# Performance work log

Measured on AMD Instinct MI355X. Metric: run time of the kernel, lower is better.

The kernel has to match this reference:

```python
import jax, jax.numpy as jnp
import numpy as np
import math

B, L = 4, 2048
D_MODEL, N_HEADS, D_K, D_V, D_FF, FACTOR = 512, 8, 64, 64, 2048, 5


def _layernorm(x, g, b, eps=1e-5):
    m = x.mean(-1, keepdims=True)
    v = jnp.mean((x - m) ** 2, axis=-1, keepdims=True)
    return (x - m) * jax.lax.rsqrt(v + eps) * g + b


def setup_inputs() -> dict:
    key = jax.random.key(0)
    ks = jax.random.split(key, 8)
    w = lambda k, shape: (jax.random.normal(k, shape, jnp.float32) * 0.02)
    sample_k = min(FACTOR * int(math.ceil(math.log(L))), L)  # c*ln(L_K) sampled keys per query
    return {
        "x": jax.random.normal(ks[0], (B, L, D_MODEL), jnp.float32),
        "Wq": w(ks[1], (D_MODEL, N_HEADS * D_K)),
        "Wk": w(ks[2], (D_MODEL, N_HEADS * D_K)),
        "Wv": w(ks[3], (D_MODEL, N_HEADS * D_V)),
        "Wo": w(ks[4], (N_HEADS * D_V, D_MODEL)),
        "ln1_g": jnp.ones((D_MODEL,), jnp.float32),
        "ln1_b": jnp.zeros((D_MODEL,), jnp.float32),
        "conv1_w": w(ks[5], (D_FF, D_MODEL)),
        "conv1_b": jnp.zeros((D_FF,), jnp.float32),
        "conv2_w": w(ks[6], (D_MODEL, D_FF)),
        "conv2_b": jnp.zeros((D_MODEL,), jnp.float32),
        "ln2_g": jnp.ones((D_MODEL,), jnp.float32),
        "ln2_b": jnp.zeros((D_MODEL,), jnp.float32),
        # Informer samples sample_k random keys per query position (constant indices)
        "sample_idx": jax.random.randint(ks[7], (L, sample_k), 0, L),
    }


def reference(x, Wq, Wk, Wv, Wo, ln1_g, ln1_b, conv1_w, conv1_b, conv2_w, conv2_b, ln2_g, ln2_b, sample_idx):
    Bx, Lx, D = x.shape
    H = N_HEADS
    # projections -> [B,H,L,d]
    Q = (x @ Wq).reshape(Bx, Lx, H, D_K).transpose(0, 2, 1, 3)
    K = (x @ Wk).reshape(Bx, Lx, H, D_K).transpose(0, 2, 1, 3)
    V = (x @ Wv).reshape(Bx, Lx, H, D_V).transpose(0, 2, 1, 3)

    u = min(FACTOR * int(math.ceil(math.log(Lx))), Lx)  # top-u active queries
    # sampled QK scores: [B,H,L,sample_k]
    K_samp = K[:, :, sample_idx]                              # [B,H,L,S,dk]
    qk_s = jnp.einsum('bhle,bhlse->bhls', Q, K_samp)
    # sparsity measure M = max - mean (Informer divides sum by L_K)
    M = qk_s.max(-1) - qk_s.sum(-1) / Lx                      # [B,H,L]
    _, top = jax.lax.top_k(M, u)                              # [B,H,u]

    Q_red = jnp.take_along_axis(Q, top[..., None], axis=2)    # [B,H,u,dk]
    scores = jnp.einsum('bhue,bhle->bhul', Q_red, K) / math.sqrt(D_K)
    attn = jax.nn.softmax(scores, axis=-1)                    # [B,H,u,L]

    # initial context = mean of V over keys; update only top-u query rows
    ctx = jnp.broadcast_to(V.mean(axis=2, keepdims=True), V.shape)  # [B,H,L,dv]
    upd = jnp.einsum('bhul,bhld->bhud', attn, V)              # [B,H,u,dv]
    bi = jnp.arange(Bx)[:, None, None]
    hi = jnp.arange(H)[None, :, None]
    ctx = ctx.at[bi, hi, top].set(upd)

    out = ctx.transpose(0, 2, 1, 3).reshape(Bx, Lx, H * D_V) @ Wo
    x1 = _layernorm(x + out, ln1_g, ln1_b)  # residual + norm inside attention sublayer

    # conv1d(k=1) FFN == per-token linear; dropout is identity in eval
    y = jax.nn.gelu(x1 @ conv1_w.T + conv1_b, approximate=False)
    y = y @ conv2_w.T + conv2_b
    return _layernorm(x1 + y, ln2_g, ln2_b)
```

## Files before the change

### kernel.cpp

```cpp
#include <hip/hip_runtime.h>
#include <hip/hip_bf16.h>

#define BB 4
#define LL 2048
#define DD 512
#define HH 8
#define DKK 64
#define FF 2048

typedef __bf16  bf16x8  __attribute__((ext_vector_type(8)));
typedef float   floatx4 __attribute__((ext_vector_type(4)));

__device__ __forceinline__ void async_cp16(const void* g, void* l) {
    __builtin_amdgcn_global_load_lds(
        (const __attribute__((address_space(1))) unsigned int*)g,
        (__attribute__((address_space(3))) unsigned int*)l,
        16, 0, 0);
}

__device__ __forceinline__ float gelu_f(float v) {
    float z  = v * 0.70710678118654752f;
    float az = fabsf(z);
    float t  = __builtin_amdgcn_rcpf(1.0f + 0.3275911f * az);
    float p  = ((((1.061405429f * t - 1.453152027f) * t + 1.421413741f) * t
                 - 0.284496736f) * t + 0.254829592f) * t;
    float e  = __expf(-z * z);
    float er = 1.0f - p * e;
    er = (z < 0.0f) ? -er : er;
    return 0.5f * v * (1.0f + er);
}

__global__ __launch_bounds__(256) void prep_w(
    const float* __restrict__ Wq, const float* __restrict__ Wk,
    const float* __restrict__ Wv, const float* __restrict__ Wo,
    __bf16* __restrict__ wb)
{
    const size_t SZ = (size_t)DD * DD;
    int z = blockIdx.z;
    const float* s = (z == 0) ? Wq : (z == 1) ? Wk : (z == 2) ? Wv : Wo;
    __bf16* hi; __bf16* lo = nullptr;
    if (z == 0)      { hi = wb;          lo = wb + SZ; }
    else if (z == 1) { hi = wb + 2 * SZ; lo = wb + 3 * SZ; }
    else if (z == 2) { hi = wb + 4 * SZ; }
    else             { hi = wb + 5 * SZ; }
    int idx = blockIdx.x * 256 + threadIdx.x;
    int k = idx >> 9, n = idx & 511;
    float v = s[idx];
    __bf16 h = (__bf16)v;
    hi[(size_t)n * DD + k] = h;
    if (lo) lo[(size_t)n * DD + k] = (__bf16)(v - (float)h);
}

__global__ __launch_bounds__(256) void cast_cw(
    const float* __restrict__ c1w, const float* __restrict__ c2w,
    __bf16* __restrict__ d1, __bf16* __restrict__ d2)
{
    const float* s = blockIdx.z ? c2w : c1w;
    __bf16* d = blockIdx.z ? d2 : d1;
    int idx = blockIdx.x * 256 + threadIdx.x;
    d[idx] = (__bf16)s[idx];
}

__global__ __launch_bounds__(256) void split_cast_x(
    const float* __restrict__ x, __bf16* __restrict__ xhi, __bf16* __restrict__ xlo)
{
    int idx = blockIdx.x * 256 + threadIdx.x;
    float v = x[idx];
    __bf16 h = (__bf16)v;
    xhi[idx] = h;
    xlo[idx] = (__bf16)(v - (float)h);
}

template<int NB, int ACT, bool BIAS, bool OUT_BF16>
__global__ __launch_bounds__(256) void gemm_mfma(
    const __bf16* __restrict__ A, const __bf16* __restrict__ B,
    const float* __restrict__ bias, void* __restrict__ Cv,
    int M, int N, int K)
{
    __shared__ __bf16 As[NB][128 * 32];
    __shared__ __bf16 Bs[NB][128 * 32];
    const int tid = threadIdx.x;
    const int wave = tid >> 6, lane = tid & 63;
    const int gx = gridDim.x;
    const int nwg = gx * gridDim.y;
    const int hw = blockIdx.y * gx + blockIdx.x;
    const int virt = ((nwg & 7) == 0) ? ((hw & 7) * (nwg >> 3) + (hw >> 3)) : hw;
    const int m0 = (virt / gx) * 128, n0 = (virt % gx) * 128;
    const int wm = (wave >> 1) * 64, wn = (wave & 1) * 64;
    const int l15 = lane & 15, kq = lane >> 4;

    auto stage = [&](int buf, int k0) {
        #pragma unroll
        for (int p = 0; p < 2; p++) {
            int c = p * 256 + tid;
            int row = c >> 2;
            int col = ((c & 3) ^ ((row >> 1) & 3)) * 8;
            async_cp16(A + (size_t)(m0 + row) * K + k0 + col, &As[buf][c * 8]);
            async_cp16(B + (size_t)(n0 + row) * K + k0 + col, &Bs[buf][c * 8]);
        }
    };

    floatx4 acc[4][4] = {};

    const int nt = K >> 5;
    #pragma unroll
    for (int pt = 0; pt < NB - 1; pt++) stage(pt, pt << 5);
    if constexpr (NB == 6) asm volatile("s_waitcnt vmcnt(16)" ::: "memory");
    else                   asm volatile("s_waitcnt vmcnt(4)"  ::: "memory");
    __builtin_amdgcn_s_barrier();
    int bi = 0;
    for (int t = 0; t < nt; t++) {
        if (t + NB - 1 < nt) {
            int b2 = bi + NB - 1; if (b2 >= NB) b2 -= NB;
            stage(b2, (t + NB - 1) << 5);
        }
        asm volatile("" ::: "memory");
        bf16x8 af[4], bfr[4];
        #pragma unroll
        for (int i = 0; i < 4; i++) {
            int ra = wm + i * 16 + l15;
            af[i] = *(const bf16x8*)(&As[bi][ra * 32 + ((kq ^ ((ra >> 1) & 3)) << 3)]);
        }
        #pragma unroll
        for (int j = 0; j < 4; j++) {
            int rb = wn + j * 16 + l15;
            bfr[j] = *(const bf16x8*)(&Bs[bi][rb * 32 + ((kq ^ ((rb >> 1) & 3)) << 3)]);
        }
        #pragma unroll
        for (int i = 0; i < 4; i++)
            #pragma unroll
            for (int j = 0; j < 4; j++)
                acc[i][j] = __builtin_amdgcn_mfma_f32_16x16x32_bf16(bfr[j], af[i], acc[i][j], 0, 0, 0);
        asm volatile("" ::: "memory");
        if (t + 1 < nt) {
            int c = nt - 2 - t; if (c > NB - 2) c = NB - 2;
            if (c >= 4)      asm volatile("s_waitcnt vmcnt(16)" ::: "memory");
            else if (c == 3) asm volatile("s_waitcnt vmcnt(12)" ::: "memory");
            else if (c == 2) asm volatile("s_waitcnt vmcnt(8)"  ::: "memory");
            else if (c == 1) asm volatile("s_waitcnt vmcnt(4)"  ::: "memory");
            else             asm volatile("s_waitcnt vmcnt(0)"  ::: "memory");
            __builtin_amdgcn_s_barrier();
        }
        if (++bi == NB) bi = 0;
    }
    #pragma unroll
    for (int i = 0; i < 4; i++) {
        int m = m0 + wm + i * 16 + l15;
        #pragma unroll
        for (int j = 0; j < 4; j++) {
            int n = n0 + wn + j * 16 + kq * 4;
            floatx4 v4 = acc[i][j];
            if (BIAS) {
                float4 bv = *(const float4*)&bias[n];
                v4[0] += bv.x; v4[1] += bv.y; v4[2] += bv.z; v4[3] += bv.w;
            }
            if (ACT == 1) {
                v4[0] = gelu_f(v4[0]); v4[1] = gelu_f(v4[1]);
                v4[2] = gelu_f(v4[2]); v4[3] = gelu_f(v4[3]);
            }
            if (OUT_BF16) {
                union { __bf16 b[4]; uint2 u; } pk;
                pk.b[0] = (__bf16)v4[0]; pk.b[1] = (__bf16)v4[1];
                pk.b[2] = (__bf16)v4[2]; pk.b[3] = (__bf16)v4[3];
                *(uint2*)((__bf16*)Cv + (size_t)m * N + n) = pk.u;
            } else {
                *(float4*)((float*)Cv + (size_t)m * N + n) = *(float4*)&v4;
            }
        }
    }
}

template<int NB, int ACT, bool BIAS, bool OUT_BF16>
__global__ __launch_bounds__(256) void gemm_sq64(
    const __bf16* __restrict__ A, const __bf16* __restrict__ B,
    const float* __restrict__ bias, void* __restrict__ Cv,
    int M, int N, int K)
{
    __shared__ __bf16 As[NB][64 * 32];
    __shared__ __bf16 Bs[NB][64 * 32];
    const int tid = threadIdx.x;
    const int wave = tid >> 6, lane = tid & 63;
    const int gx = gridDim.x;
    const int nwg = gx * gridDim.y;
    const int hw = blockIdx.y * gx + blockIdx.x;
    const int virt = ((nwg & 7) == 0) ? ((hw & 7) * (nwg >> 3) + (hw >> 3)) : hw;
    const int m0 = (virt / gx) * 64, n0 = (virt % gx) * 64;
    const int wm = (wave >> 1) * 32, wn = (wave & 1) * 32;
    const int l15 = lane & 15, kq = lane >> 4;

    auto stage = [&](int buf, int k0) {
        int c = tid;
        int row = c >> 2;
        int col = ((c & 3) ^ ((row >> 1) & 3)) * 8;
        async_cp16(A + (size_t)(m0 + row) * K + k0 + col, &As[buf][c * 8]);
        async_cp16(B + (size_t)(n0 + row) * K + k0 + col, &Bs[buf][c * 8]);
    };

    floatx4 acc[2][2] = {};

    const int nt = K >> 5;
    #pragma unroll
    for (int pt = 0; pt < NB - 1; pt++) stage(pt, pt << 5);
    asm volatile("s_waitcnt vmcnt(%0)" :: "i"(2 * (NB - 2)) : "memory");
    __builtin_amdgcn_s_barrier();
    int bi = 0;
    for (int t = 0; t < nt; t++) {
        if (t + NB - 1 < nt) {
            int b2 = bi + NB - 1; if (b2 >= NB) b2 -= NB;
            stage(b2, (t + NB - 1) << 5);
        }
        asm volatile("" ::: "memory");
        bf16x8 af[2], bfr[2];
        #pragma unroll
        for (int i = 0; i < 2; i++) {
            int ra = wm + i * 16 + l15;
            af[i] = *(const bf16x8*)(&As[bi][ra * 32 + ((kq ^ ((ra >> 1) & 3)) << 3)]);
        }
        #pragma unroll
        for (int j = 0; j < 2; j++) {
            int rb = wn + j * 16 + l15;
            bfr[j] = *(const bf16x8*)(&Bs[bi][rb * 32 + ((kq ^ ((rb >> 1) & 3)) << 3)]);
        }
        #pragma unroll
        for (int i = 0; i < 2; i++)
            #pragma unroll
            for (int j = 0; j < 2; j++)
                acc[i][j] = __builtin_amdgcn_mfma_f32_16x16x32_bf16(bfr[j], af[i], acc[i][j], 0, 0, 0);
        asm volatile("" ::: "memory");
        if (t + 1 < nt) {
            int c = nt - 2 - t; if (c > NB - 2) c = NB - 2;
            if (c >= 3)      asm volatile("s_waitcnt vmcnt(6)" ::: "memory");
            else if (c == 2) asm volatile("s_waitcnt vmcnt(4)" ::: "memory");
            else if (c == 1) asm volatile("s_waitcnt vmcnt(2)" ::: "memory");
            else             asm volatile("s_waitcnt vmcnt(0)" ::: "memory");
            __builtin_amdgcn_s_barrier();
        }
        if (++bi == NB) bi = 0;
    }
    #pragma unroll
    for (int i = 0; i < 2; i++) {
        int m = m0 + wm + i * 16 + l15;
        #pragma unroll
        for (int j = 0; j < 2; j++) {
            int n = n0 + wn + j * 16 + kq * 4;
            floatx4 v4 = acc[i][j];
            if (BIAS) {
                float4 bv = *(const float4*)&bias[n];
                v4[0] += bv.x; v4[1] += bv.y; v4[2] += bv.z; v4[3] += bv.w;
            }
            if (ACT == 1) {
                v4[0] = gelu_f(v4[0]); v4[1] = gelu_f(v4[1]);
                v4[2] = gelu_f(v4[2]); v4[3] = gelu_f(v4[3]);
            }
            if (OUT_BF16) {
                union { __bf16 b[4]; uint2 u; } pk;
                pk.b[0] = (__bf16)v4[0]; pk.b[1] = (__bf16)v4[1];
                pk.b[2] = (__bf16)v4[2]; pk.b[3] = (__bf16)v4[3];
                *(uint2*)((__bf16*)Cv + (size_t)m * N + n) = pk.u;
            } else {
                *(float4*)((float*)Cv + (size_t)m * N + n) = *(float4*)&v4;
            }
        }
    }
}

__global__ __launch_bounds__(256) void gemm_mfma_split64(
    const __bf16* __restrict__ Ah, const __bf16* __restrict__ Al,
    const __bf16* __restrict__ Bh, const __bf16* __restrict__ Bl,
    float* __restrict__ C, int M, int N, int K)
{
    __shared__ __bf16 Ahs[3][64 * 32];
    __shared__ __bf16 Als[3][64 * 32];
    __shared__ __bf16 Bhs[3][128 * 32];
    __shared__ __bf16 Bls[3][128 * 32];
    const int tid = threadIdx.x;
    const int wave = tid >> 6, lane = tid & 63;
    const int gx = gridDim.x;
    const int nwg = gx * gridDim.y;
    const int hw = blockIdx.y * gx + blockIdx.x;
    const int virt = ((nwg & 7) == 0) ? ((hw & 7) * (nwg >> 3) + (hw >> 3)) : hw;
    const int m0 = (virt / gx) * 64, n0 = (virt % gx) * 128;
    const int wm = (wave >> 1) * 32, wn = (wave & 1) * 64;
    const int l15 = lane & 15, kq = lane >> 4;

    auto stage = [&](int buf, int k0) {
        {
            int c = tid;
            int row = c >> 2;
            int col = ((c & 3) ^ ((row >> 1) & 3)) * 8;
            size_t go = (size_t)(m0 + row) * K + k0 + col;
            async_cp16(Ah + go, &Ahs[buf][c * 8]);
            async_cp16(Al + go, &Als[buf][c * 8]);
        }
        #pragma unroll
        for (int p = 0; p < 2; p++) {
            int c = p * 256 + tid;
            int row = c >> 2;
            int col = ((c & 3) ^ ((row >> 1) & 3)) * 8;
            size_t go = (size_t)(n0 + row) * K + k0 + col;
            async_cp16(Bh + go, &Bhs[buf][c * 8]);
            async_cp16(Bl + go, &Bls[buf][c * 8]);
        }
    };

    floatx4 acc[2][4] = {};

    const int nt = K >> 5;
    stage(0, 0); stage(1, 32);
    asm volatile("s_waitcnt vmcnt(6)" ::: "memory");
    __builtin_amdgcn_s_barrier();
    int bi = 0;
    for (int t = 0; t < nt; t++) {
        if (t + 2 < nt) {
            int b2 = bi + 2; if (b2 >= 3) b2 -= 3;
            stage(b2, (t + 2) << 5);
        }
        asm volatile("" ::: "memory");
        bf16x8 ah[2], al[2], bh[4], bl[4];
        #pragma unroll
        for (int i = 0; i < 2; i++) {
            int ra = wm + i * 16 + l15;
            int off = ra * 32 + ((kq ^ ((ra >> 1) & 3)) << 3);
            ah[i] = *(const bf16x8*)(&Ahs[bi][off]);
            al[i] = *(const bf16x8*)(&Als[bi][off]);
        }
        #pragma unroll
        for (int j = 0; j < 4; j++) {
            int rb = wn + j * 16 + l15;
            int off = rb * 32 + ((kq ^ ((rb >> 1) & 3)) << 3);
            bh[j] = *(const bf16x8*)(&Bhs[bi][off]);
            bl[j] = *(const bf16x8*)(&Bls[bi][off]);
        }
        #pragma unroll
        for (int i = 0; i < 2; i++)
            #pragma unroll
            for (int j = 0; j < 4; j++) {
                acc[i][j] = __builtin_amdgcn_mfma_f32_16x16x32_bf16(bh[j], ah[i], acc[i][j], 0, 0, 0);
                acc[i][j] = __builtin_amdgcn_mfma_f32_16x16x32_bf16(bl[j], ah[i], acc[i][j], 0, 0, 0);
                acc[i][j] = __builtin_amdgcn_mfma_f32_16x16x32_bf16(bh[j], al[i], acc[i][j], 0, 0, 0);
            }
        asm volatile("" ::: "memory");
        if (t + 1 < nt) {
            if (t + 2 < nt) asm volatile("s_waitcnt vmcnt(6)" ::: "memory");
            else            asm volatile("s_waitcnt vmcnt(0)" ::: "memory");
            __builtin_amdgcn_s_barrier();
        }
        if (++bi == 3) bi = 0;
    }
    #pragma unroll
    for (int i = 0; i < 2; i++) {
        int m = m0 + wm + i * 16 + l15;
        #pragma unroll
        for (int j = 0; j < 4; j++) {
            int n = n0 + wn + j * 16 + kq * 4;
            *(float4*)(C + (size_t)m * N + n) = *(float4*)&acc[i][j];
        }
    }
}

__device__ __forceinline__ float dpp_sum16(float p) {
    int t;
    t = __builtin_amdgcn_update_dpp(0, __float_as_int(p), 0xB1,  0xF, 0xF, true);
    p += __int_as_float(t);
    t = __builtin_amdgcn_update_dpp(0, __float_as_int(p), 0x4E,  0xF, 0xF, true);
    p += __int_as_float(t);
    t = __builtin_amdgcn_update_dpp(0, __float_as_int(p), 0x141, 0xF, 0xF, true);
    p += __int_as_float(t);
    t = __builtin_amdgcn_update_dpp(0, __float_as_int(p), 0x140, 0xF, 0xF, true);
    p += __int_as_float(t);
    return p;
}

__global__ __launch_bounds__(256) void calc_m(
    const float* __restrict__ Q, const float* __restrict__ Kb,
    const int* __restrict__ sidx, float* __restrict__ Mo, int U)
{
    __shared__ int   js[64];
    __shared__ float red_mx[2][HH];
    __shared__ float red_sm[2][HH];
    int i = blockIdx.x;
    int b = i & 3, l = i >> 2;
    int tid = threadIdx.x;
    if (tid < U) js[tid] = sidx[l * U + tid];
    int e    = (tid & 127) * 4;
    int slot = tid >> 7;
    const float* qr = Q + ((size_t)(b * LL + l) * DD);
    float4 q = *(const float4*)(qr + e);
    const float* kbase = Kb + ((size_t)b * LL) * DD + e;
    __syncthreads();
    float mx = -1e30f, sm = 0.f;
    for (int s = slot; s < U; s += 2) {
        int j = js[s];
        float4 kv = *(const float4*)(kbase + (size_t)j * DD);
        float p = q.x * kv.x + q.y * kv.y + q.z * kv.z + q.w * kv.w;
        p = dpp_sum16(p);
        mx = fmaxf(mx, p);
        sm += p;
    }
    if ((tid & 15) == 0) {
        int head = (tid >> 4) & 7;
        red_mx[slot][head] = mx;
        red_sm[slot][head] = sm;
    }
    __syncthreads();
    if (tid < HH) {
        float m2 = fmaxf(red_mx[0][tid], red_mx[1][tid]);
        float s2 = red_sm[0][tid] + red_sm[1][tid];
        Mo[((size_t)(b * HH + tid)) * LL + l] = m2 - s2 * (1.0f / (float)LL);
    }
}

__global__ __launch_bounds__(256) void topk_k(
    const float* __restrict__ Mo, int* __restrict__ top, int U)
{
    __shared__ unsigned int hist[256];
    __shared__ unsigned int wsum[4];
    __shared__ unsigned int bc[2];
    __shared__ int ties[LL];
    __shared__ int cnt2[2];
    int bh = blockIdx.x, tid = threadIdx.x;
    int lane = tid & 63, w = tid >> 6;

    unsigned int my[8];
    #pragma unroll
    for (int i = 0; i < 8; i++) {
        unsigned int u = __float_as_uint(Mo[(size_t)bh * LL + tid + i * 256]);
        my[i] = u ^ ((u >> 31) ? 0xFFFFFFFFu : 0x80000000u);
    }

    unsigned int prefix = 0, pmask = 0;
    unsigned int need = (unsigned int)U;
    unsigned int above = 0;

    for (int pass = 0; pass < 4; pass++) {
        int shift = 24 - pass * 8;
        hist[tid] = 0;
        __syncthreads();
        #pragma unroll
        for (int i = 0; i < 8; i++) {
            unsigned int u = my[i];
            if ((u & pmask) == prefix)
                atomicAdd(&hist[(u >> shift) & 255u], 1u);
        }
        __syncthreads();
        unsigned int h = hist[tid];
        #pragma unroll
        for (int off = 1; off < 64; off <<= 1) {
            unsigned int o = __shfl_down(h, off);
            if (lane + off < 64) h += o;
        }
        if (lane == 0) wsum[w] = h;
        __syncthreads();
        unsigned int tail = 0;
        #pragma unroll
        for (int w2 = 1; w2 < 4; w2++) if (w2 > w) tail += wsum[w2];
        h += tail;
        hist[tid] = h;
        __syncthreads();
        unsigned int St = h;
        unsigned int St1 = (tid < 255) ? hist[tid + 1] : 0u;
        if (St >= need && St1 < need) { bc[0] = (unsigned int)tid; bc[1] = St1; }
        __syncthreads();
        unsigned int dig = bc[0], abv = bc[1];
        above += abv;
        need -= abv;
        prefix |= dig << shift;
        pmask |= 0xFFu << shift;
        __syncthreads();
    }

    if (tid == 0) { cnt2[0] = 0; cnt2[1] = 0; }
    __syncthreads();
    #pragma unroll
    for (int i = 0; i < 8; i++) {
        unsigned int u = my[i];
        int idx = tid + i * 256;
        if (u > prefix) {
            int pos = atomicAdd(&cnt2[0], 1);
            top[bh * U + pos] = idx;
        } else if (u == prefix) {
            int pos = atomicAdd(&cnt2[1], 1);
            ties[pos] = idx;
        }
    }
    __syncthreads();
    int tcnt = cnt2[1];
    #pragma unroll
    for (int i = 0; i < 8; i++) {
        unsigned int u = my[i];
        if (u == prefix) {
            int idx = tid + i * 256;
            int rank = 0;
            for (int j = 0; j < tcnt; j++) rank += (ties[j] < idx) ? 1 : 0;
            if (rank < (int)need) top[bh * U + (int)above + rank] = idx;
        }
    }
}

__global__ __launch_bounds__(256) void vmean_k(
    const __bf16* __restrict__ V, float* __restrict__ Vm)
{
    __shared__ float osum[4][DKK];
    int bh = blockIdx.x;
    int b = bh >> 3, h = bh & 7;
    int tid = threadIdx.x, d = tid & 63, part = tid >> 6;
    const __bf16* vp = V + ((size_t)(b * LL + part * 512) * DD + h * DKK + d);
    float s = 0.f;
    for (int i = 0; i < 512; i++) s += (float)vp[(size_t)i * DD];
    osum[part][d] = s;
    __syncthreads();
    if (tid < DKK)
        Vm[bh * DKK + tid] = (osum[0][tid] + osum[1][tid] + osum[2][tid] + osum[3][tid]) * (1.0f / (float)LL);
}

__global__ __launch_bounds__(256) void gather_qred(
    const float* __restrict__ Q, const int* __restrict__ top,
    __bf16* __restrict__ qred, int U)
{
    int bh = blockIdx.y;
    int b = bh >> 3, h = bh & 7;
    int e = blockIdx.x * 256 + threadIdx.x;
    int u = e >> 6, d = e & 63;
    float v = 0.f;
    if (u < U) {
        int l = top[bh * U + u];
        v = Q[((size_t)(b * LL + l) * DD + h * DKK) + d] * 0.125f;
    }
    qred[(size_t)bh * 48 * DKK + e] = (__bf16)v;
}

__global__ __launch_bounds__(256) void gemm_s(
    const __bf16* __restrict__ qred, const float* __restrict__ Kb,
    float* __restrict__ S)
{
    __shared__ __bf16 Qs[2 * 48 * 32];
    __shared__ __bf16 Ks[2 * 128 * 32];
    int bh = blockIdx.y, nc = blockIdx.x;
    int b = bh >> 3, h = bh & 7, l0 = nc * 128;
    int tid = threadIdx.x;
    const unsigned int* qsrc = (const unsigned int*)(qred + (size_t)bh * 48 * DKK);
    unsigned int* qdst = (unsigned int*)Qs;
    #pragma unroll
    for (int t = 0; t < 6; t++) {
        int ui = tid + t * 256;
        int u = ui >> 5, kp = ui & 31;
        int p = kp >> 4, kl2 = kp & 15;
        qdst[p * 768 + u * 16 + kl2] = qsrc[ui];
    }
    #pragma unroll
    for (int t = 0; t < 8; t++) {
        int fi = tid + t * 256;
        int row = fi >> 4, k4 = fi & 15;
        int p = k4 >> 3, kl = (k4 & 7) * 4;
        float4 kv = *(const float4*)(Kb + ((size_t)(b * LL + l0 + row) * DD + h * DKK + k4 * 4));
        __bf16* dst = Ks + p * 128 * 32 + row * 32 + kl;
        dst[0] = (__bf16)kv.x; dst[1] = (__bf16)kv.y;
        dst[2] = (__bf16)kv.z; dst[3] = (__bf16)kv.w;
    }
    __syncthreads();
    int wave = tid >> 6, lane = tid & 63, l15 = lane & 15, kq = lane >> 4;
    floatx4 acc[3][2] = {};
    #pragma unroll
    for (int p = 0; p < 2; p++) {
        bf16x8 bq[2];
        #pragma unroll
        for (int j = 0; j < 2; j++)
            bq[j] = *(const bf16x8*)(Ks + p * 4096 + (wave * 32 + j * 16 + l15) * 32 + kq * 8);
        #pragma unroll
        for (int i = 0; i < 3; i++) {
            bf16x8 aq = *(const bf16x8*)(Qs + p * 1536 + (i * 16 + l15) * 32 + kq * 8);
            #pragma unroll
            for (int j = 0; j < 2; j++)
                acc[i][j] = __builtin_amdgcn_mfma_f32_16x16x32_bf16(bq[j], aq, acc[i][j], 0, 0, 0);
        }
    }
    #pragma unroll
    for (int i = 0; i < 3; i++) {
        int row = i * 16 + l15;
        #pragma unroll
        for (int j = 0; j < 2; j++) {
            int col = l0 + wave * 32 + j * 16 + kq * 4;
            *(float4*)&S[((size_t)bh * 48 + row) * LL + col] = *(float4*)&acc[i][j];
        }
    }
}

__global__ __launch_bounds__(256) void softmax_p(float* __restrict__ S, int U)
{
    __shared__ float red[256];
    int row = blockIdx.x;
    int bh = row / U, u = row % U;
    float* sr = S + ((size_t)bh * 48 + u) * LL;
    int tid = threadIdx.x;
    float sc[8]; float mx = -1e30f;
    #pragma unroll
    for (int i = 0; i < 8; i++) { sc[i] = sr[tid + i * 256]; mx = fmaxf(mx, sc[i]); }
    red[tid] = mx; __syncthreads();
    for (int s = 128; s > 0; s >>= 1) { if (tid < s) red[tid] = fmaxf(red[tid], red[tid + s]); __syncthreads(); }
    mx = red[0]; __syncthreads();
    float se = 0.f;
    #pragma unroll
    for (int i = 0; i < 8; i++) { sc[i] = __expf(sc[i] - mx); se += sc[i]; }
    red[tid] = se; __syncthreads();
    for (int s = 128; s > 0; s >>= 1) { if (tid < s) red[tid] += red[tid + s]; __syncthreads(); }
    float inv = 1.0f / red[0];
    __bf16* pr = (__bf16*)sr;
    #pragma unroll
    for (int i = 0; i < 8; i++) pr[tid + i * 256] = (__bf16)(sc[i] * inv);
}

__global__ __launch_bounds__(256) void zero_upd(float* __restrict__ upd, int n)
{
    int i = blockIdx.x * 256 + threadIdx.x;
    if (i < n) upd[i] = 0.f;
}

__global__ __launch_bounds__(256) void pv_k(
    const float* __restrict__ S, const __bf16* __restrict__ V,
    float* __restrict__ upd, int U)
{
    __shared__ __bf16 pls[4][512];
    __shared__ float osum[16][4][DKK];
    int uc = blockIdx.x, lc = blockIdx.y, bh = blockIdx.z;
    int b = bh >> 3, h = bh & 7, tid = threadIdx.x;
    #pragma unroll
    for (int t = 0; t < 4; t++) {
        int ui = tid + t * 256;
        int up = ui >> 8, lw = ui & 255;
        ((unsigned int*)pls)[up * 256 + lw] =
            ((const unsigned int*)(S + ((size_t)bh * 48 + uc * 4 + up) * LL))[lc * 256 + lw];
    }
    __syncthreads();
    int d4 = tid & 15, part = tid >> 4;
    const __bf16* vp = V + ((size_t)(b * LL + lc * 512 + part * 32)) * DD + h * DKK + d4 * 4;
    float a[4][4] = {};
    for (int i = 0; i < 32; i++) {
        union { uint2 u; __bf16 bb[4]; } cv;
        cv.u = *(const uint2*)(vp + (size_t)i * DD);
        float v0 = (float)cv.bb[0], v1 = (float)cv.bb[1];
        float v2 = (float)cv.bb[2], v3 = (float)cv.bb[3];
        int l = part * 32 + i;
        #pragma unroll
        for (int u2 = 0; u2 < 4; u2++) {
            float p = (float)pls[u2][l];
            a[u2][0] += p * v0; a[u2][1] += p * v1;
            a[u2][2] += p * v2; a[u2][3] += p * v3;
        }
    }
    #pragma unroll
    for (int u2 = 0; u2 < 4; u2++)
        #pragma unroll
        for (int j = 0; j < 4; j++)
            osum[part][u2][d4 * 4 + j] = a[u2][j];
    __syncthreads();
    int d = tid & 63, u2 = tid >> 6;
    float s = 0.f;
    #pragma unroll
    for (int p = 0; p < 16; p++) s += osum[p][u2][d];
    atomicAdd(&upd[((size_t)bh * U + uc * 4 + u2) * DKK + d], s);
}

__global__ __launch_bounds__(256) void base_k(
    const float* __restrict__ Vm, const float* __restrict__ Wo,
    float* __restrict__ base)
{
    __shared__ float cm[DD];
    __shared__ float part[8][32];
    int b = blockIdx.y, n0 = blockIdx.x * 32, tid = threadIdx.x;
    cm[tid] = Vm[b * DD + tid];
    cm[tid + 256] = Vm[b * DD + 256 + tid];
    __syncthreads();
    int n = n0 + (tid & 31), kg = tid >> 5;
    float s = 0.f;
    for (int k = kg * 64; k < kg * 64 + 64; k++) s += cm[k] * Wo[(size_t)k * DD + n];
    part[kg][tid & 31] = s;
    __syncthreads();
    if (tid < 32) {
        float t = 0.f;
        #pragma unroll
        for (int g = 0; g < 8; g++) t += part[g][tid];
        base[b * DD + n0 + tid] = t;
    }
}

__global__ __launch_bounds__(256) void aout_init(
    const float* __restrict__ base, float* __restrict__ aout)
{
    int idx = blockIdx.x * 256 + threadIdx.x;
    aout[idx] = base[((idx >> 20) << 9) + (idx & 511)];
}

__global__ __launch_bounds__(256) void aw_prep(
    const float* __restrict__ upd, const float* __restrict__ Vm,
    __bf16* __restrict__ aw, int U)
{
    int bh = blockIdx.x, tid = threadIdx.x;
    #pragma unroll
    for (int t = 0; t < 12; t++) {
        int e = tid + t * 256;
        int u = e >> 6, d = e & 63;
        float v = (u < U) ? upd[((size_t)bh * U + u) * DKK + d] - Vm[bh * DKK + d] : 0.f;
        aw[(size_t)bh * 48 * DKK + e] = (__bf16)v;
    }
}

__global__ __launch_bounds__(256) void corr_gemm(
    const __bf16* __restrict__ aw, const __bf16* __restrict__ WoT,
    const int* __restrict__ top, float* __restrict__ aout, int U)
{
    __shared__ __bf16 Qs[2 * 48 * 32];
    __shared__ __bf16 Ks[2 * 128 * 32];
    int bh = blockIdx.y, nc = blockIdx.x;
    int b = bh >> 3, h = bh & 7, n0 = nc * 128;
    int tid = threadIdx.x;
    const unsigned int* qsrc = (const unsigned int*)(aw + (size_t)bh * 48 * DKK);
    unsigned int* qdst = (unsigned int*)Qs;
    #pragma unroll
    for (int t = 0; t < 6; t++) {
        int ui = tid + t * 256;
        int u = ui >> 5, kp = ui & 31;
        int p = kp >> 4, kl2 = kp & 15;
        qdst[p * 768 + u * 16 + kl2] = qsrc[ui];
    }
    const unsigned int* wsrc = (const unsigned int*)WoT;
    unsigned int* kdst = (unsigned int*)Ks;
    #pragma unroll
    for (int t = 0; t < 16; t++) {
        int ui = tid + t * 256;
        int row = ui >> 5, c2 = ui & 31;
        int p = c2 >> 4, col2 = c2 & 15;
        kdst[p * 2048 + row * 16 + col2] = wsrc[(size_t)(n0 + row) * (DD / 2) + h * 32 + c2];
    }
    __syncthreads();
    int wave = tid >> 6, lane = tid & 63, l15 = lane & 15, kq = lane >> 4;
    floatx4 acc[3][2] = {};
    #pragma unroll
    for (int p = 0; p < 2; p++) {
        bf16x8 bq[2];
        #pragma unroll
        for (int j = 0; j < 2; j++)
            bq[j] = *(const bf16x8*)(Ks + p * 4096 + (wave * 32 + j * 16 + l15) * 32 + kq * 8);
        #pragma unroll
        for (int i = 0; i < 3; i++) {
            bf16x8 aq = *(const bf16x8*)(Qs + p * 1536 + (i * 16 + l15) * 32 + kq * 8);
            #pragma unroll
            for (int j = 0; j < 2; j++)
                acc[i][j] = __builtin_amdgcn_mfma_f32_16x16x32_bf16(bq[j], aq, acc[i][j], 0, 0, 0);
        }
    }
    #pragma unroll
    for (int i = 0; i < 3; i++) {
        int u = i * 16 + l15;
        if (u < U) {
            int l = top[bh * U + u];
            float* dst = aout + ((size_t)(b * LL + l)) * DD;
            #pragma unroll
            for (int j = 0; j < 2; j++) {
                int n = n0 + wave * 32 + j * 16 + kq * 4;
                atomicAdd(dst + n,     acc[i][j][0]);
                atomicAdd(dst + n + 1, acc[i][j][1]);
                atomicAdd(dst + n + 2, acc[i][j][2]);
                atomicAdd(dst + n + 3, acc[i][j][3]);
            }
        }
    }
}

__global__ __launch_bounds__(256) void ln1_k(
    const float* __restrict__ x, const float* __restrict__ aout,
    const float* __restrict__ g, const float* __restrict__ bb,
    __bf16* __restrict__ x1h)
{
    __shared__ float red[256];
    int row = blockIdx.x, tid = threadIdx.x;
    size_t base = (size_t)row * DD;
    float h0 = x[base + tid] + aout[base + tid];
    float h1 = x[base + 256 + tid] + aout[base + 256 + tid];
    red[tid] = h0 + h1; __syncthreads();
    for (int s = 128; s > 0; s >>= 1) { if (tid < s) red[tid] += red[tid + s]; __syncthreads(); }
    float mean = red[0] * (1.0f / DD); __syncthreads();
    float d0 = h0 - mean, d1 = h1 - mean;
    red[tid] = d0 * d0 + d1 * d1; __syncthreads();
    for (int s = 128; s > 0; s >>= 1) { if (tid < s) red[tid] += red[tid + s]; __syncthreads(); }
    float rstd = rsqrtf(red[0] * (1.0f / DD) + 1e-5f);
    x1h[base + tid]       = (__bf16)(d0 * rstd * g[tid] + bb[tid]);
    x1h[base + 256 + tid] = (__bf16)(d1 * rstd * g[256 + tid] + bb[256 + tid]);
}

__global__ __launch_bounds__(256) void ln2_k(
    const __bf16* __restrict__ x1h, const float* __restrict__ f2o,
    const float* __restrict__ c2b,
    const float* __restrict__ g, const float* __restrict__ bb,
    float* __restrict__ out)
{
    __shared__ float red[256];
    int row = blockIdx.x, tid = threadIdx.x;
    size_t base = (size_t)row * DD;
    float h0 = (float)x1h[base + tid] + f2o[base + tid] + c2b[tid];
    float h1 = (float)x1h[base + 256 + tid] + f2o[base + 256 + tid] + c2b[256 + tid];
    red[tid] = h0 + h1; __syncthreads();
    for (int s = 128; s > 0; s >>= 1) { if (tid < s) red[tid] += red[tid + s]; __syncthreads(); }
    float mean = red[0] * (1.0f / DD); __syncthreads();
    float d0 = h0 - mean, d1 = h1 - mean;
    red[tid] = d0 * d0 + d1 * d1; __syncthreads();
    for (int s = 128; s > 0; s >>= 1) { if (tid < s) red[tid] += red[tid + s]; __syncthreads(); }
    float rstd = rsqrtf(red[0] * (1.0f / DD) + 1e-5f);
    out[base + tid]       = d0 * rstd * g[tid] + bb[tid];
    out[base + 256 + tid] = d1 * rstd * g[256 + tid] + bb[256 + tid];
}

extern "C" void kernel_launch(void* const* d_in, const int* in_sizes, int n_in,
                              void* d_out, int out_size, void* d_ws, size_t ws_size,
                              hipStream_t stream)
{
    const float* x   = (const float*)d_in[0];
    const float* Wq  = (const float*)d_in[1];
    const float* Wk  = (const float*)d_in[2];
    const float* Wv  = (const float*)d_in[3];
    const float* Wo  = (const float*)d_in[4];
    const float* g1  = (const float*)d_in[5];
    const float* b1  = (const float*)d_in[6];
    const float* c1w = (const float*)d_in[7];
    const float* c1b = (const float*)d_in[8];
    const float* c2w = (const float*)d_in[9];
    const float* c2b = (const float*)d_in[10];
    const float* g2  = (const float*)d_in[11];
    const float* b2  = (const float*)d_in[12];
    const int* sidx  = (const int*)d_in[13];
    float* out       = (float*)d_out;

    const int U = in_sizes[13] / LL;
    const int M = BB * LL;

    char* ws = (char*)d_ws;
    const size_t MB = (size_t)1 << 20;
    float*  Q    = (float*)(ws + 0);
    float*  Kb   = (float*)(ws + 16 * MB);
    __bf16* V    = (__bf16*)(ws + 32 * MB);
    __bf16* xhi  = (__bf16*)(ws + 40 * MB);
    __bf16* xlo  = (__bf16*)(ws + 48 * MB);
    float*  S    = (float*)(ws + 40 * MB);
    __bf16* wb   = (__bf16*)(ws + 56 * MB);
    __bf16* c1wb = (__bf16*)(ws + 59 * MB);
    __bf16* c2wb = (__bf16*)(ws + 61 * MB);
    float*  Mo   = (float*)(ws + 63 * MB);
    float*  upd  = (float*)(ws + 63 * MB + 256 * 1024);
    float*  Vm   = (float*)(ws + 63 * MB + 576 * 1024);
    int*    top  = (int*)  (ws + 63 * MB + 584 * 1024);
    __bf16* qred = (__bf16*)(ws + 63 * MB + 592 * 1024);
    __bf16* aw   = (__bf16*)(ws + 63 * MB + 784 * 1024);
    float*  basep= (float*)(ws + 63 * MB + 976 * 1024);
    float*  aout = Q;
    float*  f2o  = Q;
    __bf16* ych  = (__bf16*)(ws + 16 * MB);
    __bf16* x1h  = xlo;
    (void)ws_size; (void)n_in; (void)out_size;

    const size_t SZ = (size_t)DD * DD;
    __bf16* WqThi = wb;          __bf16* WqTlo = wb + SZ;
    __bf16* WkThi = wb + 2 * SZ; __bf16* WkTlo = wb + 3 * SZ;
    __bf16* WvT   = wb + 4 * SZ; __bf16* WoT   = wb + 5 * SZ;

    prep_w<<<dim3(DD * DD / 256, 1, 4), 256, 0, stream>>>(Wq, Wk, Wv, Wo, wb);
    cast_cw<<<dim3(FF * DD / 256, 1, 2), 256, 0, stream>>>(c1w, c2w, c1wb, c2wb);
    split_cast_x<<<BB * LL * DD / 256, 256, 0, stream>>>(x, xhi, xlo);

    dim3 gproj64(DD / 128, M / 64);
    gemm_mfma_split64<<<gproj64, 256, 0, stream>>>(xhi, xlo, WqThi, WqTlo, Q,  M, DD, DD);
    gemm_mfma_split64<<<gproj64, 256, 0, stream>>>(xhi, xlo, WkThi, WkTlo, Kb, M, DD, DD);
    dim3 gsq(DD / 64, M / 64);
    gemm_sq64<4, 0, false, true ><<<gsq, 256, 0, stream>>>(xhi, WvT, nullptr, V, M, DD, DD);

    calc_m<<<BB * LL, 256, 0, stream>>>(Q, Kb, sidx, Mo, U);
    zero_upd<<<(BB * HH * U * DKK + 255) / 256, 256, 0, stream>>>(upd, BB * HH * U * DKK);
    topk_k<<<BB * HH, 256, 0, stream>>>(Mo, top, U);
    vmean_k<<<BB * HH, 256, 0, stream>>>(V, Vm);

    gather_qred<<<dim3(48 * DKK / 256, BB * HH), 256, 0, stream>>>(Q, top, qred, U);
    gemm_s<<<dim3(LL / 128, BB * HH), 256, 0, stream>>>(qred, Kb, S);
    softmax_p<<<BB * HH * U, 256, 0, stream>>>(S, U);
    pv_k<<<dim3(U / 4, 4, BB * HH), 256, 0, stream>>>(S, V, upd, U);

    base_k<<<dim3(16, BB), 256, 0, stream>>>(Vm, Wo, basep);
    aw_prep<<<BB * HH, 256, 0, stream>>>(upd, Vm, aw, U);
    aout_init<<<M * DD / 256, 256, 0, stream>>>(basep, aout);
    corr_gemm<<<dim3(DD / 128, BB * HH), 256, 0, stream>>>(aw, WoT, top, aout, U);

    ln1_k<<<M, 256, 0, stream>>>(x, aout, g1, b1, x1h);

    gemm_mfma<3, 1, true,  true ><<<dim3(FF / 128, M / 128), 256, 0, stream>>>(x1h, c1wb, c1b, ych, M, FF, DD);
    gemm_sq64<4, 0, false, false><<<gsq, 256, 0, stream>>>(ych, c2wb, nullptr, f2o, M, DD, FF);

    ln2_k<<<M, 256, 0, stream>>>(x1h, f2o, c2b, g2, b2, out);
}
```

Baseline: 384.6 us.

## Fuse Q and K split-precision projections into one GEMM with 64x64 tiles

```diff
diff --git a/kernel.cpp b/kernel.cpp
--- a/kernel.cpp
+++ b/kernel.cpp
@@ -39,8 +39,8 @@
     int z = blockIdx.z;
     const float* s = (z == 0) ? Wq : (z == 1) ? Wk : (z == 2) ? Wv : Wo;
     __bf16* hi; __bf16* lo = nullptr;
-    if (z == 0)      { hi = wb;          lo = wb + SZ; }
-    else if (z == 1) { hi = wb + 2 * SZ; lo = wb + 3 * SZ; }
+    if (z == 0)      { hi = wb;          lo = wb + 2 * SZ; }
+    else if (z == 1) { hi = wb + SZ;     lo = wb + 3 * SZ; }
     else if (z == 2) { hi = wb + 4 * SZ; }
     else             { hi = wb + 5 * SZ; }
     int idx = blockIdx.x * 256 + threadIdx.x;
@@ -105,8 +105,7 @@
     const int nt = K >> 5;
     #pragma unroll
     for (int pt = 0; pt < NB - 1; pt++) stage(pt, pt << 5);
-    if constexpr (NB == 6) asm volatile("s_waitcnt vmcnt(16)" ::: "memory");
-    else                   asm volatile("s_waitcnt vmcnt(4)"  ::: "memory");
+    asm volatile("s_waitcnt vmcnt(4)"  ::: "memory");
     __builtin_amdgcn_s_barrier();
     int bi = 0;
     for (int t = 0; t < nt; t++) {
@@ -134,9 +133,7 @@
         asm volatile("" ::: "memory");
         if (t + 1 < nt) {
             int c = nt - 2 - t; if (c > NB - 2) c = NB - 2;
-            if (c >= 4)      asm volatile("s_waitcnt vmcnt(16)" ::: "memory");
-            else if (c == 3) asm volatile("s_waitcnt vmcnt(12)" ::: "memory");
-            else if (c == 2) asm volatile("s_waitcnt vmcnt(8)"  ::: "memory");
+            if (c >= 2)      asm volatile("s_waitcnt vmcnt(8)"  ::: "memory");
             else if (c == 1) asm volatile("s_waitcnt vmcnt(4)"  ::: "memory");
             else             asm volatile("s_waitcnt vmcnt(0)"  ::: "memory");
             __builtin_amdgcn_s_barrier();
@@ -264,59 +261,48 @@
     }
 }
 
-__global__ __launch_bounds__(256) void gemm_mfma_split64(
+__global__ __launch_bounds__(256) void gemm_split_qk(
     const __bf16* __restrict__ Ah, const __bf16* __restrict__ Al,
     const __bf16* __restrict__ Bh, const __bf16* __restrict__ Bl,
-    float* __restrict__ C, int M, int N, int K)
-{
-    __shared__ __bf16 Ahs[3][64 * 32];
-    __shared__ __bf16 Als[3][64 * 32];
-    __shared__ __bf16 Bhs[3][128 * 32];
-    __shared__ __bf16 Bls[3][128 * 32];
+    float* __restrict__ Cq, float* __restrict__ Ck, int M, int K)
+{
+    __shared__ __bf16 Ahs[2][64 * 32];
+    __shared__ __bf16 Als[2][64 * 32];
+    __shared__ __bf16 Bhs[2][64 * 32];
+    __shared__ __bf16 Bls[2][64 * 32];
     const int tid = threadIdx.x;
     const int wave = tid >> 6, lane = tid & 63;
     const int gx = gridDim.x;
     const int nwg = gx * gridDim.y;
     const int hw = blockIdx.y * gx + blockIdx.x;
     const int virt = ((nwg & 7) == 0) ? ((hw & 7) * (nwg >> 3) + (hw >> 3)) : hw;
-    const int m0 = (virt / gx) * 64, n0 = (virt % gx) * 128;
-    const int wm = (wave >> 1) * 32, wn = (wave & 1) * 64;
+    const int m0 = (virt / gx) * 64, n0 = (virt % gx) * 64;
+    const int wm = (wave >> 1) * 32, wn = (wave & 1) * 32;
     const int l15 = lane & 15, kq = lane >> 4;
 
     auto stage = [&](int buf, int k0) {
-        {
-            int c = tid;
-            int row = c >> 2;
-            int col = ((c & 3) ^ ((row >> 1) & 3)) * 8;
-            size_t go = (size_t)(m0 + row) * K + k0 + col;
-            async_cp16(Ah + go, &Ahs[buf][c * 8]);
-            async_cp16(Al + go, &Als[buf][c * 8]);
-        }
-        #pragma unroll
-        for (int p = 0; p < 2; p++) {
-            int c = p * 256 + tid;
-            int row = c >> 2;
-            int col = ((c & 3) ^ ((row >> 1) & 3)) * 8;
-            size_t go = (size_t)(n0 + row) * K + k0 + col;
-            async_cp16(Bh + go, &Bhs[buf][c * 8]);
-            async_cp16(Bl + go, &Bls[buf][c * 8]);
-        }
+        int c = tid;
+        int row = c >> 2;
+        int col = ((c & 3) ^ ((row >> 1) & 3)) * 8;
+        size_t goA = (size_t)(m0 + row) * K + k0 + col;
+        size_t goB = (size_t)(n0 + row) * K + k0 + col;
+        async_cp16(Ah + goA, &Ahs[buf][c * 8]);
+        async_cp16(Al + goA, &Als[buf][c * 8]);
+        async_cp16(Bh + goB, &Bhs[buf][c * 8]);
+        async_cp16(Bl + goB, &Bls[buf][c * 8]);
     };
 
-    floatx4 acc[2][4] = {};
+    floatx4 acc[2][2] = {};
 
     const int nt = K >> 5;
-    stage(0, 0); stage(1, 32);
-    asm volatile("s_waitcnt vmcnt(6)" ::: "memory");
+    stage(0, 0);
+    asm volatile("s_waitcnt vmcnt(0)" ::: "memory");
     __builtin_amdgcn_s_barrier();
     int bi = 0;
     for (int t = 0; t < nt; t++) {
-        if (t + 2 < nt) {
-            int b2 = bi + 2; if (b2 >= 3) b2 -= 3;
-            stage(b2, (t + 2) << 5);
-        }
+        if (t + 1 < nt) stage(bi ^ 1, (t + 1) << 5);
         asm volatile("" ::: "memory");
-        bf16x8 ah[2], al[2], bh[4], bl[4];
+        bf16x8 ah[2], al[2], bh[2], bl[2];
         #pragma unroll
         for (int i = 0; i < 2; i++) {
             int ra = wm + i * 16 + l15;
@@ -325,7 +311,7 @@
             al[i] = *(const bf16x8*)(&Als[bi][off]);
         }
         #pragma unroll
-        for (int j = 0; j < 4; j++) {
+        for (int j = 0; j < 2; j++) {
             int rb = wn + j * 16 + l15;
             int off = rb * 32 + ((kq ^ ((rb >> 1) & 3)) << 3);
             bh[j] = *(const bf16x8*)(&Bhs[bi][off]);
@@ -334,26 +320,27 @@
         #pragma unroll
         for (int i = 0; i < 2; i++)
             #pragma unroll
-            for (int j = 0; j < 4; j++) {
+            for (int j = 0; j < 2; j++) {
                 acc[i][j] = __builtin_amdgcn_mfma_f32_16x16x32_bf16(bh[j], ah[i], acc[i][j], 0, 0, 0);
                 acc[i][j] = __builtin_amdgcn_mfma_f32_16x16x32_bf16(bl[j], ah[i], acc[i][j], 0, 0, 0);
                 acc[i][j] = __builtin_amdgcn_mfma_f32_16x16x32_bf16(bh[j], al[i], acc[i][j], 0, 0, 0);
             }
         asm volatile("" ::: "memory");
         if (t + 1 < nt) {
-            if (t + 2 < nt) asm volatile("s_waitcnt vmcnt(6)" ::: "memory");
-            else            asm volatile("s_waitcnt vmcnt(0)" ::: "memory");
+            asm volatile("s_waitcnt vmcnt(0)" ::: "memory");
             __builtin_amdgcn_s_barrier();
         }
-        if (++bi == 3) bi = 0;
-    }
+        bi ^= 1;
+    }
+    float* C = (n0 < DD) ? Cq : Ck;
+    const int nc0 = n0 & (DD - 1);
     #pragma unroll
     for (int i = 0; i < 2; i++) {
         int m = m0 + wm + i * 16 + l15;
         #pragma unroll
-        for (int j = 0; j < 4; j++) {
-            int n = n0 + wn + j * 16 + kq * 4;
-            *(float4*)(C + (size_t)m * N + n) = *(float4*)&acc[i][j];
+        for (int j = 0; j < 2; j++) {
+            int n = nc0 + wn + j * 16 + kq * 4;
+            *(float4*)(C + (size_t)m * DD + n) = *(float4*)&acc[i][j];
         }
     }
 }
@@ -857,17 +844,17 @@
     (void)ws_size; (void)n_in; (void)out_size;
 
     const size_t SZ = (size_t)DD * DD;
-    __bf16* WqThi = wb;          __bf16* WqTlo = wb + SZ;
-    __bf16* WkThi = wb + 2 * SZ; __bf16* WkTlo = wb + 3 * SZ;
-    __bf16* WvT   = wb + 4 * SZ; __bf16* WoT   = wb + 5 * SZ;
+    __bf16* WqkHi = wb;
+    __bf16* WqkLo = wb + 2 * SZ;
+    __bf16* WvT   = wb + 4 * SZ;
+    __bf16* WoT   = wb + 5 * SZ;
 
     prep_w<<<dim3(DD * DD / 256, 1, 4), 256, 0, stream>>>(Wq, Wk, Wv, Wo, wb);
     cast_cw<<<dim3(FF * DD / 256, 1, 2), 256, 0, stream>>>(c1w, c2w, c1wb, c2wb);
     split_cast_x<<<BB * LL * DD / 256, 256, 0, stream>>>(x, xhi, xlo);
 
-    dim3 gproj64(DD / 128, M / 64);
-    gemm_mfma_split64<<<gproj64, 256, 0, stream>>>(xhi, xlo, WqThi, WqTlo, Q,  M, DD, DD);
-    gemm_mfma_split64<<<gproj64, 256, 0, stream>>>(xhi, xlo, WkThi, WkTlo, Kb, M, DD, DD);
+    dim3 gqk((2 * DD) / 64, M / 64);
+    gemm_split_qk<<<gqk, 256, 0, stream>>>(xhi, xlo, WqkHi, WqkLo, Q, Kb, M, DD);
     dim3 gsq(DD / 64, M / 64);
     gemm_sq64<4, 0, false, true ><<<gsq, 256, 0, stream>>>(xhi, WvT, nullptr, V, M, DD, DD);
 
```

Result: no change. 380.4 us (-1.1%).
